# Kernel optimization log

Hardware: AMD Instinct MI355X
Metric: run time of the kernel (lower is better)

## Reference

```python
import jax, jax.numpy as jnp
import numpy as np
import math

H = 8
D_MODEL = 32
D_HEAD = 4
FACTOR = 5
EPS = 1e-5

DATANUM = 1024
B = 512            # outer batch; becomes attention sequence length
C = 32
L = DATANUM // 8   # 128; becomes attention batch
U = min(FACTOR * int(math.ceil(math.log(B))), B)  # 35 (U_part == u since L_Q == L_K == B)


def setup_inputs() -> dict:
    key = jax.random.key(0)
    ks = jax.random.split(key, 16)
    s = 0.05
    return {
        'x': jax.random.normal(ks[0], (B, C, L), jnp.float32),
        'Wq': jax.random.normal(ks[1], (D_MODEL, D_MODEL), jnp.float32) * s,
        'bq': jnp.zeros((D_MODEL,), jnp.float32),
        'Wk': jax.random.normal(ks[2], (D_MODEL, D_MODEL), jnp.float32) * s,
        'bk': jnp.zeros((D_MODEL,), jnp.float32),
        'Wv': jax.random.normal(ks[3], (D_MODEL, D_MODEL), jnp.float32) * s,
        'bv': jnp.zeros((D_MODEL,), jnp.float32),
        'Wo': jax.random.normal(ks[4], (D_MODEL, D_MODEL), jnp.float32) * s,
        'bo': jnp.zeros((D_MODEL,), jnp.float32),
        'bn1_gamma': jnp.ones((C,), jnp.float32),
        'bn1_beta': jnp.zeros((C,), jnp.float32),
        'bn1_mean': jnp.zeros((C,), jnp.float32),
        'bn1_var': jnp.ones((C,), jnp.float32),
        'W1': jax.random.normal(ks[5], (DATANUM * 8, DATANUM * 4), jnp.float32) * 0.01,
        'b1': jnp.zeros((DATANUM * 8,), jnp.float32),
        'W2': jax.random.normal(ks[6], (DATANUM * 4, DATANUM * 8), jnp.float32) * 0.01,
        'b2': jnp.zeros((DATANUM * 4,), jnp.float32),
        'bn2_gamma': jnp.ones((C,), jnp.float32),
        'bn2_beta': jnp.zeros((C,), jnp.float32),
        'bn2_mean': jnp.zeros((C,), jnp.float32),
        'bn2_var': jnp.ones((C,), jnp.float32),
        'index_sample': jax.random.randint(ks[7], (B, U), 0, B, jnp.int64),
    }


def _bn(x, gamma, beta, mean, var):
    # eval-mode BatchNorm1d over channel dim of (batch, C, length)
    inv = jax.lax.rsqrt(var + EPS)
    return (x - mean[None, :, None]) * (inv * gamma)[None, :, None] + beta[None, :, None]


def _prob_attention(Q, K, V, index_sample):
    # Q,K,V: (Ba, H, Lq, D) self-attention, Lq == Lk. Informer ProbAttention, mask_flag=True.
    Ba, Hh, Lq, D = Q.shape
    u = index_sample.shape[1]
    # sparsity measurement on sampled keys
    K_sample = K[:, :, index_sample, :]                       # (Ba,H,Lq,U,D)
    QK_sample = jnp.einsum('bhld,bhlud->bhlu', Q, K_sample)
    M = QK_sample.max(axis=-1) - QK_sample.sum(axis=-1) / Lq  # (Ba,H,Lq)
    _, M_top = jax.lax.top_k(M, u)                            # (Ba,H,u) selected queries
    Q_reduce = jnp.take_along_axis(Q, M_top[..., None], axis=2)  # (Ba,H,u,D)
    scores = jnp.einsum('bhud,bhkd->bhuk', Q_reduce, K) / jnp.sqrt(jnp.float32(D))
    # ProbMask: causal w.r.t. the selected query's original position
    causal = jnp.arange(Lq)[None, None, None, :] > M_top[..., None]
    scores = jnp.where(causal, -jnp.inf, scores)
    attn = jax.nn.softmax(scores, axis=-1)
    upd = jnp.einsum('bhuk,bhkd->bhud', attn, V)              # (Ba,H,u,D)
    context = jnp.cumsum(V, axis=2)                           # initial context (mask_flag=True)
    b_idx = jnp.arange(Ba)[:, None, None]
    h_idx = jnp.arange(Hh)[None, :, None]
    context = context.at[b_idx, h_idx, M_top].set(upd)
    return context


def reference(x, Wq, bq, Wk, bk, Wv, bv, Wo, bo,
              bn1_gamma, bn1_beta, bn1_mean, bn1_var,
              W1, b1, W2, b2,
              bn2_gamma, bn2_beta, bn2_mean, bn2_var,
              index_sample):
    Bsz, Cc, Ll = x.shape
    res1 = x
    xa = jnp.transpose(x, (2, 0, 1))                          # (L, B, 32): attn batch=L, seq=B

    def heads(t):
        return jnp.transpose(t.reshape(Ll, Bsz, H, D_HEAD), (0, 2, 1, 3))

    Q = heads(xa @ Wq.T + bq)
    K = heads(xa @ Wk.T + bk)
    V = heads(xa @ Wv.T + bv)
    ctx = _prob_attention(Q, K, V, index_sample)              # (L,H,B,D)
    out = jnp.transpose(ctx, (0, 2, 1, 3)).reshape(Ll, Bsz, D_MODEL)
    out = out @ Wo.T + bo
    xh = jax.nn.relu(out)                                     # dropout = identity (eval)
    xh = jnp.transpose(xh, (1, 2, 0))                         # (B,32,L)
    xh = _bn(xh + res1, bn1_gamma, bn1_beta, bn1_mean, bn1_var)
    res2 = xh
    f = xh.reshape(Bsz, Cc * Ll)
    f = jax.nn.relu(f @ W1.T + b1)
    f = jax.nn.relu(f @ W2.T + b2)
    f = f.reshape(Bsz, Cc, Ll)
    return _bn(f + res2, bn2_gamma, bn2_beta, bn2_mean, bn2_var)
```

## Files before the change

kernel.cpp:

```cpp
#include <hip/hip_runtime.h>
#include <stdint.h>

#define EPSF 1e-5f
#define NEG_INF (-1e30f)

typedef float f32x4 __attribute__((ext_vector_type(4)));
typedef __bf16 bf16x8 __attribute__((ext_vector_type(8)));
typedef unsigned short u16x8 __attribute__((ext_vector_type(8)));

typedef __attribute__((address_space(3))) unsigned char* as3_ptr;
typedef const __attribute__((address_space(1))) unsigned char* as1_ptr;

__device__ __forceinline__ void async16(const void* g, void* l) {
  __builtin_amdgcn_global_load_lds((as1_ptr)g, (as3_ptr)l, 16, 0, 0);
}

__device__ __forceinline__ unsigned short f2bf(float f) {
  union { float f; unsigned int u; } v; v.f = f;
  unsigned int r = v.u + 0x7FFFu + ((v.u >> 16) & 1u);
  return (unsigned short)(r >> 16);
}
__device__ __forceinline__ unsigned short f2bf_fast(float f) {
  union { float f; unsigned int u; } v; v.f = f;
  return (unsigned short)((v.u + 0x8000u) >> 16);
}

__global__ __launch_bounds__(256) void transpose_k(const float* __restrict__ src,
                                                   float* __restrict__ dst, int R, int C) {
  __shared__ float tl[32][33];
  int tx = threadIdx.x & 31, ty = threadIdx.x >> 5;
  int c0 = blockIdx.x * 32, r0 = blockIdx.y * 32;
#pragma unroll
  for (int i = 0; i < 4; i++)
    tl[ty + i * 8][tx] = src[(size_t)(r0 + ty + i * 8) * C + c0 + tx];
  __syncthreads();
#pragma unroll
  for (int i = 0; i < 4; i++)
    dst[(size_t)(c0 + ty + i * 8) * R + r0 + tx] = tl[tx][ty + i * 8];
}

__global__ __launch_bounds__(256) void qkv_k(const float* __restrict__ xT,
    const float* __restrict__ Wq, const float* __restrict__ bq,
    const float* __restrict__ Wk, const float* __restrict__ bk,
    const float* __restrict__ Wv, const float* __restrict__ bv,
    float* __restrict__ Q, float* __restrict__ Kq, float* __restrict__ Vq) {
  __shared__ float xs[64 * 33];
  __shared__ float wq[32 * 33], wk[32 * 33], wvs[32 * 33];
  __shared__ float bqs[32], bks[32], bvs[32];
  int tid = threadIdx.x;
  int a = blockIdx.x;
  int tbase = blockIdx.y * 256;
#pragma unroll
  for (int i = 0; i < 4; i++) {
    int e = i * 256 + tid; int r = e >> 5, c = e & 31;
    wq[r * 33 + c] = Wq[e]; wk[r * 33 + c] = Wk[e]; wvs[r * 33 + c] = Wv[e];
  }
  if (tid < 32) { bqs[tid] = bq[tid]; bks[tid] = bk[tid]; bvs[tid] = bv[tid]; }
  int tl = tid & 63, rg = tid >> 6;
  for (int ch = 0; ch < 4; ch++) {
    __syncthreads();
#pragma unroll
    for (int i = 0; i < 8; i++) {
      int e = i * 256 + tid; int r = e >> 5, c = e & 31;
      xs[r * 33 + c] = xT[(size_t)a * 16384 + (size_t)(tbase + ch * 64) * 32 + e];
    }
    __syncthreads();
    float qa[8], ka[8], va[8];
#pragma unroll
    for (int r8 = 0; r8 < 8; r8++) {
      int r = rg * 8 + r8; qa[r8] = bqs[r]; ka[r8] = bks[r]; va[r8] = bvs[r];
    }
    for (int c = 0; c < 32; c++) {
      float xv = xs[tl * 33 + c];
#pragma unroll
      for (int r8 = 0; r8 < 8; r8++) {
        int r = rg * 8 + r8;
        qa[r8] += xv * wq[r * 33 + c];
        ka[r8] += xv * wk[r * 33 + c];
        va[r8] += xv * wvs[r * 33 + c];
      }
    }
    int t = tbase + ch * 64 + tl;
#pragma unroll
    for (int r8 = 0; r8 < 8; r8++) {
      int r = rg * 8 + r8;
      size_t o = (size_t)a * 16384 + (size_t)r * 512 + t;
      Q[o] = qa[r8]; Kq[o] = ka[r8]; Vq[o] = va[r8];
    }
  }
}

__global__ __launch_bounds__(512) void topattn_k(const float* __restrict__ Q,
    const float* __restrict__ Kq, const float* __restrict__ Vq,
    const int* __restrict__ idxs, float* __restrict__ Ctx, int U) {
  __shared__ float Ks[2048];
  __shared__ float Vs[2048];
  __shared__ float Ml[512];
  __shared__ int mt[64];
  __shared__ float Qr[64][4];
  __shared__ float upd[64][4];
  int bh = blockIdx.x;
  int tid = threadIdx.x, lane = tid & 63, wv = tid >> 6;
  size_t base = (size_t)bh * 2048;
#pragma unroll
  for (int i = 0; i < 4; i++) {
    Ks[i * 512 + tid] = Kq[base + i * 512 + tid];
    Vs[i * 512 + tid] = Vq[base + i * 512 + tid];
  }
  float q0 = Q[base + tid], q1 = Q[base + 512 + tid];
  float q2 = Q[base + 1024 + tid], q3 = Q[base + 1536 + tid];
  __syncthreads();
  float mx = NEG_INF, sm = 0.f;
  for (int u = 0; u < U; u++) {
    int it = idxs[tid * U + u];
    it = min(max(it, 0), 511);
    float s = q0 * Ks[it] + q1 * Ks[512 + it] + q2 * Ks[1024 + it] + q3 * Ks[1536 + it];
    mx = fmaxf(mx, s); sm += s;
  }
  Ml[tid] = mx - sm * (1.f / 512.f);
  __syncthreads();
  float mi = Ml[tid];
  int rank = 0;
  for (int j0 = 0; j0 < 512; j0 += 4) {
    float4 m4 = *(const float4*)(Ml + j0);
    rank += (m4.x > mi) || (m4.x == mi && (j0 + 0) < tid);
    rank += (m4.y > mi) || (m4.y == mi && (j0 + 1) < tid);
    rank += (m4.z > mi) || (m4.z == mi && (j0 + 2) < tid);
    rank += (m4.w > mi) || (m4.w == mi && (j0 + 3) < tid);
  }
  if (rank < U) mt[rank] = tid;
  __syncthreads();
  if (tid < 4 * U) { int u = tid >> 2, d = tid & 3; Qr[u][d] = Q[base + d * 512 + mt[u]]; }
  __syncthreads();
  for (int u = wv; u < U; u += 8) {
    int mrow = mt[u];
    float p0q = Qr[u][0], p1q = Qr[u][1], p2q = Qr[u][2], p3q = Qr[u][3];
    float sv[8]; float lmax = NEG_INF;
#pragma unroll
    for (int jj = 0; jj < 8; jj++) {
      int k = jj * 64 + lane;
      float s = NEG_INF;
      if (k <= mrow)
        s = 0.5f * (p0q * Ks[k] + p1q * Ks[512 + k] + p2q * Ks[1024 + k] + p3q * Ks[1536 + k]);
      sv[jj] = s; lmax = fmaxf(lmax, s);
    }
#pragma unroll
    for (int off = 32; off; off >>= 1) lmax = fmaxf(lmax, __shfl_xor(lmax, off));
    float ls = 0.f, p0 = 0.f, p1 = 0.f, p2 = 0.f, p3 = 0.f;
#pragma unroll
    for (int jj = 0; jj < 8; jj++) {
      int k = jj * 64 + lane;
      if (k <= mrow) {
        float p = __expf(sv[jj] - lmax);
        ls += p; p0 += p * Vs[k]; p1 += p * Vs[512 + k];
        p2 += p * Vs[1024 + k]; p3 += p * Vs[1536 + k];
      }
    }
#pragma unroll
    for (int off = 32; off; off >>= 1) {
      ls += __shfl_xor(ls, off); p0 += __shfl_xor(p0, off); p1 += __shfl_xor(p1, off);
      p2 += __shfl_xor(p2, off); p3 += __shfl_xor(p3, off);
    }
    if (lane == 0) {
      float inv = 1.f / ls;
      upd[u][0] = p0 * inv; upd[u][1] = p1 * inv; upd[u][2] = p2 * inv; upd[u][3] = p3 * inv;
    }
  }
  __syncthreads();
  if (wv < 4) {
    float v[8];
    int b0 = wv * 512 + lane * 8;
#pragma unroll
    for (int q = 0; q < 8; q++) v[q] = Vs[b0 + q];
#pragma unroll
    for (int q = 1; q < 8; q++) v[q] += v[q - 1];
    float x = v[7];
    for (int off = 1; off < 64; off <<= 1) {
      float y = __shfl_up(x, off);
      if (lane >= off) x += y;
    }
    float excl = x - v[7];
#pragma unroll
    for (int q = 0; q < 8; q++) Vs[b0 + q] = v[q] + excl;
  }
  __syncthreads();
  if (tid < 4 * U) { int u = tid >> 2, d = tid & 3; Vs[d * 512 + mt[u]] = upd[u][d]; }
  __syncthreads();
#pragma unroll
  for (int i = 0; i < 4; i++) Ctx[base + i * 512 + tid] = Vs[i * 512 + tid];
}

__global__ __launch_bounds__(256) void oproj_k(const float* __restrict__ Ctx,
    const float* __restrict__ Wo, const float* __restrict__ bo, float* __restrict__ Y) {
  __shared__ float cs[32 * 256];
  __shared__ float wo[32 * 33];
  __shared__ float bos[32];
  int tid = threadIdx.x;
  int a = blockIdx.x, t0 = blockIdx.y * 256;
#pragma unroll
  for (int i = 0; i < 4; i++) {
    int e = i * 256 + tid; int r = e >> 5, c = e & 31;
    wo[r * 33 + c] = Wo[e];
  }
  if (tid < 32) bos[tid] = bo[tid];
#pragma unroll
  for (int i = 0; i < 32; i++) {
    int e = i * 256 + tid; int row = e >> 8, col = e & 255;
    cs[e] = Ctx[(size_t)a * 16384 + (size_t)row * 512 + t0 + col];
  }
  __syncthreads();
  int rl = tid & 31, tw = tid >> 5;
  for (int ti = 0; ti < 32; ti++) {
    int t = ti * 8 + tw;
    float acc = bos[rl];
#pragma unroll
    for (int rp = 0; rp < 32; rp++) acc += cs[rp * 256 + t] * wo[rl * 33 + rp];
    Y[(size_t)a * 16384 + (size_t)(t0 + t) * 32 + rl] = acc;
  }
}

__global__ __launch_bounds__(256) void bn1t_k(const float* __restrict__ Y,
    const float* __restrict__ x, const float* __restrict__ g1, const float* __restrict__ be1,
    const float* __restrict__ me1, const float* __restrict__ va1,
    float* __restrict__ Xh, unsigned short* __restrict__ Fb) {
  __shared__ float tl[32][33];
  int tx = threadIdx.x & 31, ty = threadIdx.x >> 5;
  int c0 = blockIdx.x * 32;
  int r0 = blockIdx.y * 32;
#pragma unroll
  for (int i = 0; i < 4; i++)
    tl[ty + i * 8][tx] = Y[(size_t)(r0 + ty + i * 8) * 16384 + c0 + tx];
  __syncthreads();
#pragma unroll
  for (int i = 0; i < 4; i++) {
    int m = c0 + ty + i * 8;
    int a = r0 + tx;
    float v = tl[tx][ty + i * 8];
    int ch = m & 31;
    size_t oi = (size_t)m * 128 + a;
    float val = fmaxf(v, 0.f) + x[oi];
    float s = g1[ch] * rsqrtf(va1[ch] + EPSF);
    float res = (val - me1[ch]) * s + be1[ch];
    Xh[oi] = res;
    Fb[oi] = f2bf(res);
  }
}

__global__ __launch_bounds__(256) void wcvt_k(const float* __restrict__ W,
    unsigned short* __restrict__ Wb, int n4) {
  int stride = gridDim.x * 256;
  for (int idx = blockIdx.x * 256 + threadIdx.x; idx < n4; idx += stride) {
    float4 w = ((const float4*)W)[idx];
    ushort4 o;
    o.x = f2bf(w.x); o.y = f2bf(w.y); o.z = f2bf(w.z); o.w = f2bf(w.w);
    ((ushort4*)Wb)[idx] = o;
  }
}

__global__ __launch_bounds__(256, 3) void gemm_bf(
    const unsigned short* __restrict__ A, const unsigned short* __restrict__ B,
    int K, int N, int MT, int NPX, int SPLITK, float* __restrict__ P, int M) {
  __shared__ unsigned char lds[16384];
  int tid = threadIdx.x;
  int lane = tid & 63, wv = tid >> 6;
  int wm = wv >> 1, wn = wv & 1;
  int lin = blockIdx.x;
  int xcd = lin & 7, slot = lin >> 3;
  int tilesPerSp = MT * NPX;
  int sp = slot / tilesPerSp;
  int rem = slot % tilesPerSp;
  int mt = rem % MT;
  int nt = xcd * NPX + rem / MT;
  int mtile0 = mt * 128, ntile0 = nt * 128;
  int m0 = mtile0 + wm * 64, n0 = ntile0 + wn * 64;
  int frow = lane & 15, q = lane >> 4;

  int nk = K / (32 * SPLITK);
  int kbase = sp * (K / SPLITK);

  f32x4 acc[4][4];
#pragma unroll
  for (int i = 0; i < 4; i++)
#pragma unroll
    for (int j = 0; j < 4; j++) { f32x4 z = {0.f, 0.f, 0.f, 0.f}; acc[i][j] = z; }

  for (int k = 0; k < nk; k++) {
    int ks = kbase + k * 32;
#pragma unroll
    for (int i = 0; i < 2; i++) {
      int e = i * 256 + tid;
      int row = e >> 2;
      int g = (e & 3) ^ ((row >> 1) & 3);
      async16(A + (size_t)(mtile0 + row) * K + ks + g * 8, lds + i * 4096 + wv * 1024);
    }
#pragma unroll
    for (int i = 0; i < 2; i++) {
      int e = i * 256 + tid;
      int row = e >> 2;
      int g = (e & 3) ^ ((row >> 1) & 3);
      async16(B + (size_t)(ntile0 + row) * K + ks + g * 8,
              lds + 8192 + i * 4096 + wv * 1024);
    }
    __syncthreads();
    bf16x8 af[4], bfr[4];
#pragma unroll
    for (int i = 0; i < 4; i++) {
      int row = wm * 64 + i * 16 + frow;
      af[i] = *(const bf16x8*)(lds + row * 64 + ((q ^ ((row >> 1) & 3)) << 4));
    }
#pragma unroll
    for (int j = 0; j < 4; j++) {
      int row = wn * 64 + j * 16 + frow;
      bfr[j] = *(const bf16x8*)(lds + 8192 + row * 64 + ((q ^ ((row >> 1) & 3)) << 4));
    }
#pragma unroll
    for (int i = 0; i < 4; i++)
#pragma unroll
      for (int j = 0; j < 4; j++)
        acc[i][j] = __builtin_amdgcn_mfma_f32_16x16x32_bf16(af[i], bfr[j], acc[i][j], 0, 0, 0);
    __syncthreads();
  }

  float* pb = P + (size_t)sp * M * N;
#pragma unroll
  for (int i = 0; i < 4; i++)
#pragma unroll
    for (int j = 0; j < 4; j++) {
      int n = n0 + j * 16 + frow;
      int mb = m0 + i * 16 + (q << 2);
#pragma unroll
      for (int r = 0; r < 4; r++)
        pb[(size_t)(mb + r) * N + n] = acc[i][j][r];
    }
}

template <int MI, int NJ, int EPI>
__global__ __launch_bounds__(256) void gemm_ps(
    const unsigned short* __restrict__ A, const float* __restrict__ Bw,
    const float* __restrict__ bias, int K, int N, int MT, int NPX, int SPLITK,
    float* __restrict__ Pout, int M,
    unsigned short* __restrict__ Hout, const float* __restrict__ res2,
    const float* __restrict__ g2, const float* __restrict__ be2,
    const float* __restrict__ me2, const float* __restrict__ va2,
    float* __restrict__ Out) {
  constexpr int BM = MI * 32;
  constexpr int BN = NJ * 32;
  constexpr int ABYTES = BM * 32 * 2;
  constexpr int BBYTES = BN * 32 * 4;
  constexpr int SA = ABYTES / 4096;
  constexpr int SB = BBYTES / 4096;
  __shared__ unsigned char lds[ABYTES + BBYTES];
  int tid = threadIdx.x;
  int lane = tid & 63, wv = tid >> 6;
  int wm = wv >> 1, wn = wv & 1;
  int lin = blockIdx.x;
  int xcd = lin & 7, slot = lin >> 3;
  int tilesPerSp = MT * NPX;
  int sp = slot / tilesPerSp;
  int rem = slot % tilesPerSp;
  int mt = rem % MT;
  int nt = xcd * NPX + rem / MT;
  int m0 = mt * BM + wm * (BM / 2);
  int n0 = nt * BN + wn * (BN / 2);
  int frow = lane & 15, q = lane >> 4;
  int nk = K / (32 * SPLITK);
  int kbase = sp * (K / SPLITK);
  f32x4 acc[MI][NJ];
#pragma unroll
  for (int i = 0; i < MI; i++)
#pragma unroll
    for (int j = 0; j < NJ; j++) { f32x4 z = {0.f, 0.f, 0.f, 0.f}; acc[i][j] = z; }
  int mtile0 = mt * BM, ntile0 = nt * BN;
  for (int k = 0; k < nk; k++) {
    int ks = kbase + k * 32;
#pragma unroll
    for (int i = 0; i < SA; i++) {
      int e = i * 256 + tid;
      int row = e >> 2;
      int g = (e & 3) ^ ((row >> 1) & 3);
      async16(A + (size_t)(mtile0 + row) * K + ks + g * 8, lds + i * 4096 + wv * 1024);
    }
#pragma unroll
    for (int i = 0; i < SB; i++) {
      int e = i * 256 + tid;
      int row = e >> 3;
      int g = (e & 7) ^ (row & 7);
      async16(Bw + (size_t)(ntile0 + row) * K + ks + g * 4,
              lds + ABYTES + i * 4096 + wv * 1024);
    }
    __syncthreads();
    bf16x8 af[MI];
    bf16x8 bfr[NJ];
#pragma unroll
    for (int i = 0; i < MI; i++) {
      int row = wm * (BM / 2) + i * 16 + frow;
      af[i] = *(const bf16x8*)(lds + row * 64 + ((q ^ ((row >> 1) & 3)) << 4));
    }
#pragma unroll
    for (int j = 0; j < NJ; j++) {
      int row = wn * (BN / 2) + j * 16 + frow;
      const unsigned char* rb = lds + ABYTES + row * 128;
      int sw = row & 7;
      float4 w0 = *(const float4*)(rb + (((2 * q + 0) ^ sw) << 4));
      float4 w1 = *(const float4*)(rb + (((2 * q + 1) ^ sw) << 4));
      union { u16x8 u; bf16x8 b; } cv;
      cv.u[0] = f2bf_fast(w0.x); cv.u[1] = f2bf_fast(w0.y);
      cv.u[2] = f2bf_fast(w0.z); cv.u[3] = f2bf_fast(w0.w);
      cv.u[4] = f2bf_fast(w1.x); cv.u[5] = f2bf_fast(w1.y);
      cv.u[6] = f2bf_fast(w1.z); cv.u[7] = f2bf_fast(w1.w);
      bfr[j] = cv.b;
    }
#pragma unroll
    for (int i = 0; i < MI; i++)
#pragma unroll
      for (int j = 0; j < NJ; j++)
        acc[i][j] = __builtin_amdgcn_mfma_f32_16x16x32_bf16(af[i], bfr[j], acc[i][j], 0, 0, 0);
    __syncthreads();
  }
#pragma unroll
  for (int i = 0; i < MI; i++)
#pragma unroll
    for (int j = 0; j < NJ; j++) {
      int n = n0 + j * 16 + frow;
      int mb = m0 + i * 16 + (q << 2);
      if constexpr (EPI == 2) {
        float* pb = Pout + (size_t)sp * M * N;
#pragma unroll
        for (int r = 0; r < 4; r++)
          pb[(size_t)(mb + r) * N + n] = acc[i][j][r];
      } else if constexpr (EPI == 0) {
        float bb = bias[n];
#pragma unroll
        for (int r = 0; r < 4; r++) {
          float v = fmaxf(acc[i][j][r] + bb, 0.f);
          Hout[(size_t)(mb + r) * N + n] = f2bf(v);
        }
      } else {
        float bb = bias[n];
        int ch = n >> 7;
        float s = g2[ch] * rsqrtf(va2[ch] + EPSF);
        float mu = me2[ch], bt = be2[ch];
#pragma unroll
        for (int r = 0; r < 4; r++) {
          float v = fmaxf(acc[i][j][r] + bb, 0.f);
          size_t oi = (size_t)(mb + r) * N + n;
          v += res2[oi];
          Out[oi] = (v - mu) * s + bt;
        }
      }
    }
}

template <int EPI>
__global__ __launch_bounds__(256) void red_k(const float* __restrict__ P, int SP,
    const float* __restrict__ bias, const float* __restrict__ Xh,
    const float* __restrict__ g2, const float* __restrict__ be2,
    const float* __restrict__ me2, const float* __restrict__ va2,
    unsigned short* __restrict__ H, float* __restrict__ Out, int N, int MN) {
  int idx = blockIdx.x * 256 + threadIdx.x;
  const float4* p = (const float4*)P;
  int mn4 = MN >> 2;
  float4 s = p[idx];
  for (int sp = 1; sp < SP; sp++) {
    float4 t = p[idx + (size_t)sp * mn4];
    s.x += t.x; s.y += t.y; s.z += t.z; s.w += t.w;
  }
  int n = (idx << 2) & (N - 1);
  float4 bb = *(const float4*)(bias + n);
  if constexpr (EPI == 0) {
    ushort4 o;
    o.x = f2bf(fmaxf(s.x + bb.x, 0.f));
    o.y = f2bf(fmaxf(s.y + bb.y, 0.f));
    o.z = f2bf(fmaxf(s.z + bb.z, 0.f));
    o.w = f2bf(fmaxf(s.w + bb.w, 0.f));
    ((ushort4*)H)[idx] = o;
  } else {
    int ch = n >> 7;
    float sc = g2[ch] * rsqrtf(va2[ch] + EPSF);
    float mu = me2[ch], bt = be2[ch];
    float4 xh = ((const float4*)Xh)[idx];
    float4 o;
    o.x = (fmaxf(s.x + bb.x, 0.f) + xh.x - mu) * sc + bt;
    o.y = (fmaxf(s.y + bb.y, 0.f) + xh.y - mu) * sc + bt;
    o.z = (fmaxf(s.z + bb.z, 0.f) + xh.z - mu) * sc + bt;
    o.w = (fmaxf(s.w + bb.w, 0.f) + xh.w - mu) * sc + bt;
    ((float4*)Out)[idx] = o;
  }
}

extern "C" void kernel_launch(void* const* d_in, const int* in_sizes, int n_in,
                              void* d_out, int out_size, void* d_ws, size_t ws_size,
                              hipStream_t stream) {
  const float* x  = (const float*)d_in[0];
  const float* Wq = (const float*)d_in[1];  const float* bq = (const float*)d_in[2];
  const float* Wk = (const float*)d_in[3];  const float* bk = (const float*)d_in[4];
  const float* Wv = (const float*)d_in[5];  const float* bv = (const float*)d_in[6];
  const float* Wo = (const float*)d_in[7];  const float* bo = (const float*)d_in[8];
  const float* g1 = (const float*)d_in[9];  const float* be1 = (const float*)d_in[10];
  const float* me1 = (const float*)d_in[11]; const float* va1 = (const float*)d_in[12];
  const float* W1 = (const float*)d_in[13]; const float* b1 = (const float*)d_in[14];
  const float* W2 = (const float*)d_in[15]; const float* b2 = (const float*)d_in[16];
  const float* g2 = (const float*)d_in[17]; const float* be2 = (const float*)d_in[18];
  const float* me2 = (const float*)d_in[19]; const float* va2 = (const float*)d_in[20];
  const int* idxs = (const int*)d_in[21];
  int U = in_sizes[21] / 512;
  float* out = (float*)d_out;

  char* ws = (char*)d_ws;
  float* QC = (float*)(ws);
  float* Kb = (float*)(ws + (8u << 20));
  float* Vb = (float*)(ws + (16u << 20));
  float* YT = (float*)(ws + (24u << 20));
  float* Xh = (float*)(ws + (32u << 20));
  unsigned short* Fb = (unsigned short*)Vb;
  unsigned short* Hb = (unsigned short*)Kb;
  unsigned short* Wb = (unsigned short*)(ws + (48u << 20));
  float* PA = (float*)(ws + (112u << 20));
  float* P1 = (float*)(ws + (48u << 20));
  float* P2 = (float*)(ws + (80u << 20));
  bool tierA = ws_size >= (size_t)176 * (1u << 20);
  bool tierB = !tierA && ws_size >= (size_t)112 * (1u << 20);

  dim3 b256(256);
  transpose_k<<<dim3(4, 512), b256, 0, stream>>>(x, YT, 16384, 128);
  qkv_k<<<dim3(128, 2), b256, 0, stream>>>(YT, Wq, bq, Wk, bk, Wv, bv, QC, Kb, Vb);
  topattn_k<<<dim3(1024), dim3(512), 0, stream>>>(QC, Kb, Vb, idxs, QC, U);
  oproj_k<<<dim3(128, 2), b256, 0, stream>>>(QC, Wo, bo, YT);
  bn1t_k<<<dim3(512, 4), b256, 0, stream>>>(YT, x, g1, be1, me1, va1, Xh, Fb);

  if (tierA) {
    wcvt_k<<<dim3(2048), b256, 0, stream>>>(W1, Wb, (8192 * 4096) / 4);
    gemm_bf<<<dim3(1024), b256, 0, stream>>>(Fb, Wb, 4096, 8192, 4, 8, 4, PA, 512);
    red_k<0><<<dim3(4096), b256, 0, stream>>>(PA, 4, b1, nullptr, nullptr, nullptr,
                                              nullptr, nullptr, Hb, nullptr, 8192,
                                              512 * 8192);
    wcvt_k<<<dim3(2048), b256, 0, stream>>>(W2, Wb, (4096 * 8192) / 4);
    gemm_bf<<<dim3(1024), b256, 0, stream>>>(Hb, Wb, 8192, 4096, 4, 4, 8, PA, 512);
    red_k<1><<<dim3(2048), b256, 0, stream>>>(PA, 8, b2, Xh, g2, be2, me2, va2,
                                              nullptr, out, 4096, 512 * 4096);
  } else if (tierB) {
    gemm_ps<4, 2, 2><<<dim3(1024), b256, 0, stream>>>(
        Fb, W1, nullptr, 4096, 8192, 4, 16, 2, P1, 512,
        nullptr, nullptr, nullptr, nullptr, nullptr, nullptr, nullptr);
    red_k<0><<<dim3(4096), b256, 0, stream>>>(P1, 2, b1, nullptr, nullptr, nullptr,
                                              nullptr, nullptr, Hb, nullptr, 8192,
                                              512 * 8192);
    gemm_ps<4, 2, 2><<<dim3(1024), b256, 0, stream>>>(
        Hb, W2, nullptr, 8192, 4096, 4, 8, 4, P2, 512,
        nullptr, nullptr, nullptr, nullptr, nullptr, nullptr, nullptr);
    red_k<1><<<dim3(2048), b256, 0, stream>>>(P2, 4, b2, Xh, g2, be2, me2, va2,
                                              nullptr, out, 4096, 512 * 4096);
  } else {
    gemm_ps<4, 2, 0><<<dim3(512), b256, 0, stream>>>(
        Fb, W1, b1, 4096, 8192, 4, 16, 1, nullptr, 512,
        Hb, nullptr, nullptr, nullptr, nullptr, nullptr, nullptr);
    gemm_ps<4, 2, 1><<<dim3(256), b256, 0, stream>>>(
        Hb, W2, b2, 8192, 4096, 4, 8, 1, nullptr, 512,
        nullptr, Xh, g2, be2, me2, va2, out);
  }
}
```

Baseline: 553.0 us.

## Fuse fp32-to-bf16 weight conversion into GEMM LDS load path

Removes the separate weight-conversion kernels and has the GEMM load fp32 weights straight into LDS, converting them to bf16 while building MFMA fragments. This drops a full read-and-write pass over both large weight matrices and two launches. In exchange the GEMM streams twice as many weight bytes from global memory per tile and uses more LDS. Split-K is also halved with a smaller grid, and the middle workspace tier path is removed.

Result: no change. 562.3 us (+1.7%).

```diff
diff --git a/kernel.cpp b/kernel.cpp
--- a/kernel.cpp
+++ b/kernel.cpp
@@ -246,21 +246,10 @@
   }
 }
 
-__global__ __launch_bounds__(256) void wcvt_k(const float* __restrict__ W,
-    unsigned short* __restrict__ Wb, int n4) {
-  int stride = gridDim.x * 256;
-  for (int idx = blockIdx.x * 256 + threadIdx.x; idx < n4; idx += stride) {
-    float4 w = ((const float4*)W)[idx];
-    ushort4 o;
-    o.x = f2bf(w.x); o.y = f2bf(w.y); o.z = f2bf(w.z); o.w = f2bf(w.w);
-    ((ushort4*)Wb)[idx] = o;
-  }
-}
-
-__global__ __launch_bounds__(256, 3) void gemm_bf(
-    const unsigned short* __restrict__ A, const unsigned short* __restrict__ B,
+__global__ __launch_bounds__(256, 3) void gemm_fb(
+    const unsigned short* __restrict__ A, const float* __restrict__ Bw,
     int K, int N, int MT, int NPX, int SPLITK, float* __restrict__ P, int M) {
-  __shared__ unsigned char lds[16384];
+  __shared__ unsigned char lds[8192 + 16384];
   int tid = threadIdx.x;
   int lane = tid & 63, wv = tid >> 6;
   int wm = wv >> 1, wn = wv & 1;
@@ -294,11 +283,11 @@
       async16(A + (size_t)(mtile0 + row) * K + ks + g * 8, lds + i * 4096 + wv * 1024);
     }
 #pragma unroll
-    for (int i = 0; i < 2; i++) {
+    for (int i = 0; i < 4; i++) {
       int e = i * 256 + tid;
-      int row = e >> 2;
-      int g = (e & 3) ^ ((row >> 1) & 3);
-      async16(B + (size_t)(ntile0 + row) * K + ks + g * 8,
+      int row = e >> 3;
+      int g = (e & 7) ^ (row & 7);
+      async16(Bw + (size_t)(ntile0 + row) * K + ks + g * 4,
               lds + 8192 + i * 4096 + wv * 1024);
     }
     __syncthreads();
@@ -311,7 +300,14 @@
 #pragma unroll
     for (int j = 0; j < 4; j++) {
       int row = wn * 64 + j * 16 + frow;
-      bfr[j] = *(const bf16x8*)(lds + 8192 + row * 64 + ((q ^ ((row >> 1) & 3)) << 4));
+      const unsigned char* rb = lds + 8192 + row * 128;
+      int sw = row & 7;
+      float4 w0 = *(const float4*)(rb + (((2 * q + 0) ^ sw) << 4));
+      float4 w1 = *(const float4*)(rb + (((2 * q + 1) ^ sw) << 4));
+      bf16x8 b;
+      b[0] = (__bf16)w0.x; b[1] = (__bf16)w0.y; b[2] = (__bf16)w0.z; b[3] = (__bf16)w0.w;
+      b[4] = (__bf16)w1.x; b[5] = (__bf16)w1.y; b[6] = (__bf16)w1.z; b[7] = (__bf16)w1.w;
+      bfr[j] = b;
     }
 #pragma unroll
     for (int i = 0; i < 4; i++)
@@ -514,12 +510,8 @@
   float* Xh = (float*)(ws + (32u << 20));
   unsigned short* Fb = (unsigned short*)Vb;
   unsigned short* Hb = (unsigned short*)Kb;
-  unsigned short* Wb = (unsigned short*)(ws + (48u << 20));
-  float* PA = (float*)(ws + (112u << 20));
-  float* P1 = (float*)(ws + (48u << 20));
-  float* P2 = (float*)(ws + (80u << 20));
-  bool tierA = ws_size >= (size_t)176 * (1u << 20);
-  bool tierB = !tierA && ws_size >= (size_t)112 * (1u << 20);
+  float* PA = (float*)(ws + (48u << 20));
+  bool main_tier = ws_size >= (size_t)84 * (1u << 20);
 
   dim3 b256(256);
   transpose_k<<<dim3(4, 512), b256, 0, stream>>>(x, YT, 16384, 128);
@@ -528,27 +520,13 @@
   oproj_k<<<dim3(128, 2), b256, 0, stream>>>(QC, Wo, bo, YT);
   bn1t_k<<<dim3(512, 4), b256, 0, stream>>>(YT, x, g1, be1, me1, va1, Xh, Fb);
 
-  if (tierA) {
-    wcvt_k<<<dim3(2048), b256, 0, stream>>>(W1, Wb, (8192 * 4096) / 4);
-    gemm_bf<<<dim3(1024), b256, 0, stream>>>(Fb, Wb, 4096, 8192, 4, 8, 4, PA, 512);
-    red_k<0><<<dim3(4096), b256, 0, stream>>>(PA, 4, b1, nullptr, nullptr, nullptr,
+  if (main_tier) {
+    gemm_fb<<<dim3(512), b256, 0, stream>>>(Fb, W1, 4096, 8192, 4, 8, 2, PA, 512);
+    red_k<0><<<dim3(4096), b256, 0, stream>>>(PA, 2, b1, nullptr, nullptr, nullptr,
                                               nullptr, nullptr, Hb, nullptr, 8192,
                                               512 * 8192);
-    wcvt_k<<<dim3(2048), b256, 0, stream>>>(W2, Wb, (4096 * 8192) / 4);
-    gemm_bf<<<dim3(1024), b256, 0, stream>>>(Hb, Wb, 8192, 4096, 4, 4, 8, PA, 512);
-    red_k<1><<<dim3(2048), b256, 0, stream>>>(PA, 8, b2, Xh, g2, be2, me2, va2,
-                                              nullptr, out, 4096, 512 * 4096);
-  } else if (tierB) {
-    gemm_ps<4, 2, 2><<<dim3(1024), b256, 0, stream>>>(
-        Fb, W1, nullptr, 4096, 8192, 4, 16, 2, P1, 512,
-        nullptr, nullptr, nullptr, nullptr, nullptr, nullptr, nullptr);
-    red_k<0><<<dim3(4096), b256, 0, stream>>>(P1, 2, b1, nullptr, nullptr, nullptr,
-                                              nullptr, nullptr, Hb, nullptr, 8192,
-                                              512 * 8192);
-    gemm_ps<4, 2, 2><<<dim3(1024), b256, 0, stream>>>(
-        Hb, W2, nullptr, 8192, 4096, 4, 8, 4, P2, 512,
-        nullptr, nullptr, nullptr, nullptr, nullptr, nullptr, nullptr);
-    red_k<1><<<dim3(2048), b256, 0, stream>>>(P2, 4, b2, Xh, g2, be2, me2, va2,
+    gemm_fb<<<dim3(512), b256, 0, stream>>>(Hb, W2, 8192, 4096, 4, 4, 4, PA, 512);
+    red_k<1><<<dim3(2048), b256, 0, stream>>>(PA, 4, b2, Xh, g2, be2, me2, va2,
                                               nullptr, out, 4096, 512 * 4096);
   } else {
     gemm_ps<4, 2, 0><<<dim3(512), b256, 0, stream>>>(
```
